# Kernel optimization log

Measured on AMD Instinct MI355X. Metric: run time of the kernel, lower is better.

## Reference

```python
import jax, jax.numpy as jnp
import numpy as np

N, E, G = 50000, 600000, 256
D, L, V = 128, 5, 128
BN_EPS = 1e-5


def setup_inputs() -> dict:
    key = jax.random.key(0)
    ks = jax.random.split(key, 24)
    x = jax.random.randint(ks[0], (N, 9), 0, V)
    edge_index = jax.random.randint(ks[1], (2, E), 0, N)
    edge_attr = jax.random.randint(ks[2], (E, 3), 0, V)
    batch = jnp.sort(jax.random.randint(ks[3], (N,), 0, G))
    s = 0.02
    inp = dict(
        x=x, edge_index=edge_index, edge_attr=edge_attr, batch=batch,
        atom_emb=jax.random.normal(ks[4], (9, V, D)) * s,
        bond_emb=jax.random.normal(ks[5], (L, 3, V, D)) * s,
        eps=jnp.zeros((L,)),
        W1=jax.random.normal(ks[6], (D, 2 * D)) * s, b1=jnp.zeros((2 * D,)),
        g1=jnp.ones((2 * D,)), be1=jnp.zeros((2 * D,)),
        W2=jax.random.normal(ks[7], (2 * D, D)) * s, b2=jnp.zeros((D,)),
        bn_g=jnp.ones((L, D)), bn_b=jnp.zeros((L, D)),
        fcW1=jax.random.normal(ks[8], (D, 1024)) * s, fcb1=jnp.zeros((1024,)),
        fcW2=jax.random.normal(ks[9], (1024, 1024)) * s, fcb2=jnp.zeros((1024,)),
        fcW3=jax.random.normal(ks[10], (1024, 512)) * s, fcb3=jnp.zeros((512,)),
        fcW4=jax.random.normal(ks[11], (512, 1)) * s, fcb4=jnp.zeros((1,)),
    )
    return inp


def _bn(h, g, b):
    # training-mode batchnorm (biased variance, as torch uses for normalization)
    m = h.mean(0)
    v = jnp.var(h, axis=0)
    return (h - m) * jax.lax.rsqrt(v + BN_EPS) * g + b


def _embed(tables, idx):
    # tables: [F, V, D], idx: [M, F] -> sum over F of table lookups -> [M, D]
    F = tables.shape[0]
    return tables[jnp.arange(F)[None, :], idx].sum(axis=1)


def reference(x, edge_index, edge_attr, batch, atom_emb, bond_emb, eps,
              W1, b1, g1, be1, W2, b2, bn_g, bn_b,
              fcW1, fcb1, fcW2, fcb2, fcW3, fcb3, fcW4, fcb4):
    src, dst = edge_index[0], edge_index[1]

    def mlp(h):
        z = jax.nn.relu(_bn(h @ W1 + b1, g1, be1))
        return z @ W2 + b2

    h = _embed(atom_emb, x)  # AtomEncoder: [N, D]
    h_sum = h  # JK='sum' accumulator
    for l in range(L):
        e = _embed(bond_emb[l], edge_attr)            # BondEncoder: [E, D]
        msg = jax.nn.relu(h[src] + e)                  # gather + elementwise
        agg = jax.ops.segment_sum(msg, dst, num_segments=N)  # scatter-add
        h = mlp((1.0 + eps[l]) * h + agg)
        h = _bn(h, bn_g[l], bn_b[l])
        if l < L - 1:
            h = jax.nn.relu(h)
        # dropout is identity in eval mode
        h_sum = h_sum + h

    # global mean pool over graphs
    sums = jax.ops.segment_sum(h_sum, batch, num_segments=G)
    cnts = jax.ops.segment_sum(jnp.ones((N,), h_sum.dtype), batch, num_segments=G)
    rep = sums / jnp.maximum(cnts, 1.0)[:, None]

    z = jax.nn.relu(rep @ fcW1 + fcb1)
    z = jax.nn.relu(z @ fcW2 + fcb2)
    z = jax.nn.relu(z @ fcW3 + fcb3)
    out = (z @ fcW4 + fcb4).squeeze(-1)  # [G]
    return out
```

## Files before the change

kernel.cpp:

```cpp
#include <hip/hip_runtime.h>

typedef unsigned short u16;
typedef unsigned int u32;
typedef __bf16 bf16x8 __attribute__((ext_vector_type(8)));
typedef float f32x4 __attribute__((ext_vector_type(4)));
typedef float f32x2 __attribute__((ext_vector_type(2)));

#define NN 50000
#define EE 600000
#define GG 256
#define LL 5
#define NB 196

__device__ __forceinline__ float b2f(u16 u) {
  unsigned int v = ((unsigned int)u) << 16;
  return __builtin_bit_cast(float, v);
}
__device__ __forceinline__ u16 f2b(float f) {
  unsigned int u = __builtin_bit_cast(unsigned int, f);
  u += 0x7FFFu + ((u >> 16) & 1u);
  return (u16)(u >> 16);
}
__device__ __forceinline__ f32x2 up2(u32 v) {
  f32x2 r;
  r.x = __builtin_bit_cast(float, v << 16);
  r.y = __builtin_bit_cast(float, v & 0xFFFF0000u);
  return r;
}
__device__ __forceinline__ f32x2 max0(f32x2 v) {
  f32x2 r;
  r.x = fmaxf(v.x, 0.f);
  r.y = fmaxf(v.y, 0.f);
  return r;
}

__global__ void k_detect(const u32* __restrict__ w, int* __restrict__ flag) {
  __shared__ int sh[256];
  u32 v = w[threadIdx.x];
  u32 lo = v & 0xFFFFu;
  u32 e = (lo >> 7) & 0xFFu;
  sh[threadIdx.x] = (e >= 0x60u && e <= 0x7Fu) ? 1 : 0;
  __syncthreads();
  for (int s = 128; s > 0; s >>= 1) {
    if (threadIdx.x < (unsigned)s) sh[threadIdx.x] += sh[threadIdx.x + s];
    __syncthreads();
  }
  if (threadIdx.x == 0) flag[0] = (sh[0] < 128) ? 1 : 0;
}

struct CvtArgs {
  const void* src[19];
  u16* dst[19];
  int cum[20];
};

__global__ void k_cvt_all(CvtArgs a, const int* __restrict__ flag) {
  int t = blockIdx.x * 256 + threadIdx.x;
  if (t >= a.cum[19]) return;
  int i = 0;
  while (t >= a.cum[i + 1]) ++i;
  int j = t - a.cum[i];
  if (flag[0]) a.dst[i][j] = f2b(((const float*)a.src[i])[j]);
  else a.dst[i][j] = ((const u16*)a.src[i])[j];
}

__global__ void k_tr(const u16* __restrict__ src, u16* __restrict__ dst, int K, int N) {
  __shared__ u16 t[32][33];
  const int kb = blockIdx.x * 32, nb = blockIdx.y * 32;
  const int tx = threadIdx.x & 31, ty = threadIdx.x >> 5;
#pragma unroll
  for (int i = ty; i < 32; i += 8) t[i][tx] = src[(kb + i) * N + nb + tx];
  __syncthreads();
#pragma unroll
  for (int i = ty; i < 32; i += 8) dst[(nb + i) * K + kb + tx] = t[tx][i];
}

__global__ void k_init(int* __restrict__ deg, float* __restrict__ rep,
                       float* __restrict__ bnbuf, int* __restrict__ gstart,
                       int* __restrict__ gend, float* __restrict__ c1b,
                       float* __restrict__ c0b) {
  int i = blockIdx.x * 256 + threadIdx.x;
  if (i < NN) deg[i] = 0;
  if (i < GG * 128) rep[i] = 0.f;
  if (i < 768) bnbuf[i] = 0.f;
  if (i < GG) { gstart[i] = 0; gend[i] = -1; }
  if (i < 128) { c1b[i] = 1.f; c0b[i] = 0.f; }
}

__global__ void k_deg(const int* __restrict__ ei, int* __restrict__ deg) {
  int e = blockIdx.x * 256 + threadIdx.x;
  if (e < EE) atomicAdd(&deg[ei[EE + e]], 1);
}

__global__ void k_scan1(const int* __restrict__ deg, int* __restrict__ rowp,
                        int* __restrict__ bsum) {
  __shared__ int sh[256];
  int i = blockIdx.x * 256 + threadIdx.x;
  int v = (i < NN) ? deg[i] : 0;
  sh[threadIdx.x] = v;
  __syncthreads();
  for (int s = 1; s < 256; s <<= 1) {
    int t = (threadIdx.x >= (unsigned)s) ? sh[threadIdx.x - s] : 0;
    __syncthreads();
    sh[threadIdx.x] += t;
    __syncthreads();
  }
  if (i < NN) rowp[i] = sh[threadIdx.x] - v;
  if (threadIdx.x == 255) bsum[blockIdx.x] = sh[255];
}

__global__ void k_scan2(int* __restrict__ bsum, int* __restrict__ boff) {
  __shared__ int sh[256];
  int v = (threadIdx.x < NB) ? bsum[threadIdx.x] : 0;
  sh[threadIdx.x] = v;
  __syncthreads();
  for (int s = 1; s < 256; s <<= 1) {
    int t = (threadIdx.x >= (unsigned)s) ? sh[threadIdx.x - s] : 0;
    __syncthreads();
    sh[threadIdx.x] += t;
    __syncthreads();
  }
  if (threadIdx.x < NB) boff[threadIdx.x] = sh[threadIdx.x] - v;
}

__global__ void k_scan3(int* __restrict__ rowp, const int* __restrict__ boff,
                        int* __restrict__ cursor) {
  int i = blockIdx.x * 256 + threadIdx.x;
  if (i < NN) {
    int r = rowp[i] + boff[blockIdx.x];
    rowp[i] = r;
    cursor[i] = r;
  }
  if (i == 0) rowp[NN] = EE;
}

__global__ void k_fill(const int* __restrict__ ei, const int* __restrict__ eattr,
                       int* __restrict__ cursor, uint2* __restrict__ epack) {
  int e = blockIdx.x * 256 + threadIdx.x;
  if (e < EE) {
    int d = ei[EE + e];
    int pos = atomicAdd(&cursor[d], 1);
    u32 src = (u32)ei[e];
    u32 a0 = (u32)eattr[e * 3], a1 = (u32)eattr[e * 3 + 1], a2 = (u32)eattr[e * 3 + 2];
    epack[pos] = make_uint2(src | (a0 << 16) | (a1 << 23), a2);
  }
}

__global__ void k_gb(const int* __restrict__ batch, int* __restrict__ gstart,
                     int* __restrict__ gend) {
  int n = blockIdx.x * 256 + threadIdx.x;
  if (n >= NN) return;
  int b = batch[n];
  if (n == 0 || batch[n - 1] != b) gstart[b] = n;
  if (n == NN - 1 || batch[n + 1] != b) gend[b] = n;
}

__global__ void k_atom(const int* __restrict__ x, const u16* __restrict__ aemb,
                       u16* __restrict__ hpre) {
  int idx = blockIdx.x * 256 + threadIdx.x;
  if (idx >= NN * 64) return;
  int n = idx >> 6, f2 = (idx & 63) << 1;
  float a0 = 0.f, a1 = 0.f;
#pragma unroll
  for (int j = 0; j < 9; ++j) {
    int xv = x[n * 9 + j];
    u32 v = *(const u32*)(aemb + (j * 128 + xv) * 128 + f2);
    a0 += b2f((u16)v);
    a1 += b2f((u16)(v >> 16));
  }
  u32 o = (u32)f2b(a0) | ((u32)f2b(a1) << 16);
  *(u32*)(hpre + n * 128 + f2) = o;
}

__global__ __launch_bounds__(256)
void k_pull(const u16* __restrict__ hpre, const float* __restrict__ cs1,
            const float* __restrict__ cs0, int relu_h, const int* __restrict__ rowp,
            const uint2* __restrict__ epack, const u16* __restrict__ bond,
            const u16* __restrict__ epsv, int layer, u16* __restrict__ amat) {
  const int lane = threadIdx.x & 63;
  const int node = blockIdx.x * 4 + (threadIdx.x >> 6);
  const int p0 = rowp[node], p1 = rowp[node + 1];
  const int lo = lane << 1;
  const u16* bondB = bond + 16384;
  const u16* bondC = bond + 32768;
  f32x2 c1v, c0v;
  c1v.x = cs1[lo]; c1v.y = cs1[lo + 1];
  c0v.x = cs0[lo]; c0v.y = cs0[lo + 1];
  auto act = [&](u32 v) -> f32x2 {
    f32x2 t = up2(v);
    t = t * c1v + c0v;
    if (relu_h) t = max0(t);
    return t;
  };
  f32x2 acc = {0.f, 0.f};
  int p = p0;
  for (; p + 4 <= p1; p += 4) {
    uint2 e0 = epack[p], e1 = epack[p + 1], e2 = epack[p + 2], e3 = epack[p + 3];
    u32 h0 = *(const u32*)(hpre + (size_t)(e0.x & 0xFFFFu) * 128 + lo);
    u32 h1 = *(const u32*)(hpre + (size_t)(e1.x & 0xFFFFu) * 128 + lo);
    u32 h2 = *(const u32*)(hpre + (size_t)(e2.x & 0xFFFFu) * 128 + lo);
    u32 h3 = *(const u32*)(hpre + (size_t)(e3.x & 0xFFFFu) * 128 + lo);
    u32 a0 = *(const u32*)(bond + ((e0.x >> 16) & 0x7Fu) * 128 + lo);
    u32 a1 = *(const u32*)(bond + ((e1.x >> 16) & 0x7Fu) * 128 + lo);
    u32 a2 = *(const u32*)(bond + ((e2.x >> 16) & 0x7Fu) * 128 + lo);
    u32 a3 = *(const u32*)(bond + ((e3.x >> 16) & 0x7Fu) * 128 + lo);
    u32 b0 = *(const u32*)(bondB + ((e0.x >> 23) & 0x7Fu) * 128 + lo);
    u32 b1 = *(const u32*)(bondB + ((e1.x >> 23) & 0x7Fu) * 128 + lo);
    u32 b2 = *(const u32*)(bondB + ((e2.x >> 23) & 0x7Fu) * 128 + lo);
    u32 b3 = *(const u32*)(bondB + ((e3.x >> 23) & 0x7Fu) * 128 + lo);
    u32 c0 = *(const u32*)(bondC + e0.y * 128 + lo);
    u32 c1 = *(const u32*)(bondC + e1.y * 128 + lo);
    u32 c2 = *(const u32*)(bondC + e2.y * 128 + lo);
    u32 c3 = *(const u32*)(bondC + e3.y * 128 + lo);
    acc += max0(act(h0) + up2(a0) + up2(b0) + up2(c0));
    acc += max0(act(h1) + up2(a1) + up2(b1) + up2(c1));
    acc += max0(act(h2) + up2(a2) + up2(b2) + up2(c2));
    acc += max0(act(h3) + up2(a3) + up2(b3) + up2(c3));
  }
  for (; p < p1; ++p) {
    uint2 e0 = epack[p];
    u32 h0 = *(const u32*)(hpre + (size_t)(e0.x & 0xFFFFu) * 128 + lo);
    u32 a0 = *(const u32*)(bond + ((e0.x >> 16) & 0x7Fu) * 128 + lo);
    u32 b0 = *(const u32*)(bondB + ((e0.x >> 23) & 0x7Fu) * 128 + lo);
    u32 c0 = *(const u32*)(bondC + e0.y * 128 + lo);
    acc += max0(act(h0) + up2(a0) + up2(b0) + up2(c0));
  }
  float epsf = 1.0f + b2f(epsv[layer]);
  u32 own = *(const u32*)(hpre + (size_t)node * 128 + lo);
  f32x2 ow = act(own);
  u32 o = (u32)f2b(epsf * ow.x + acc.x) | ((u32)f2b(epsf * ow.y + acc.y) << 16);
  *(u32*)(amat + (size_t)node * 128 + lo) = o;
}

__global__ __launch_bounds__(256, 2)
void k_gemm1(const u16* __restrict__ amat, const u16* __restrict__ w1t,
             const u16* __restrict__ b1, u16* __restrict__ z0,
             float* __restrict__ bnsum, float* __restrict__ bnsq) {
  __shared__ u16 As[128 * 72];
  __shared__ u16 Bs[128 * 72];
  __shared__ float colAcc[256];
  const int tid = threadIdx.x;
  const int r0 = blockIdx.x * 128;
  const int nc = blockIdx.y * 128;
  const int w = tid >> 6, lane = tid & 63, l15 = lane & 15, q = lane >> 4;
  const int wr = (w & 1) * 64, wc = (w >> 1) * 64;
  f32x4 acc[4][4];
#pragma unroll
  for (int i = 0; i < 4; ++i)
#pragma unroll
    for (int j = 0; j < 4; ++j) acc[i][j] = {0.f, 0.f, 0.f, 0.f};

#pragma unroll
  for (int ks = 0; ks < 2; ++ks) {
    const int k0 = ks * 64;
    for (int idx = tid; idx < 1024; idx += 256) {
      const int row = idx >> 3, c8 = (idx & 7) << 3;
      int gr = r0 + row; if (gr >= NN) gr = NN - 1;
      uint4 va = *(const uint4*)(amat + (size_t)gr * 128 + k0 + c8);
      *(uint4*)(As + row * 72 + c8) = va;
      uint4 vb = *(const uint4*)(w1t + (size_t)(nc + row) * 128 + k0 + c8);
      *(uint4*)(Bs + row * 72 + c8) = vb;
    }
    __syncthreads();
#pragma unroll
    for (int kk = 0; kk < 64; kk += 32) {
      const int kf = kk + q * 8;
      bf16x8 a[4], b[4];
#pragma unroll
      for (int i = 0; i < 4; ++i) a[i] = *(const bf16x8*)(As + (wr + i * 16 + l15) * 72 + kf);
#pragma unroll
      for (int j = 0; j < 4; ++j) b[j] = *(const bf16x8*)(Bs + (wc + j * 16 + l15) * 72 + kf);
#pragma unroll
      for (int i = 0; i < 4; ++i)
#pragma unroll
        for (int j = 0; j < 4; ++j)
          acc[i][j] = __builtin_amdgcn_mfma_f32_16x16x32_bf16(a[i], b[j], acc[i][j], 0, 0, 0);
    }
    __syncthreads();
  }
  colAcc[tid] = 0.f;
  __syncthreads();
#pragma unroll
  for (int j = 0; j < 4; ++j) {
    const int c = wc + j * 16 + l15;
    const float bias = b2f(b1[nc + c]);
    float ls = 0.f, lsq = 0.f;
#pragma unroll
    for (int i = 0; i < 4; ++i) {
      const int gr = r0 + wr + i * 16 + q * 4;
#pragma unroll
      for (int rg = 0; rg < 4; ++rg) {
        if (gr + rg < NN) {
          const float v = acc[i][j][rg] + bias;
          z0[(gr + rg) * 256 + nc + c] = f2b(v);
          ls += v;
          lsq += v * v;
        }
      }
    }
    atomicAdd(&colAcc[c], ls);
    atomicAdd(&colAcc[128 + c], lsq);
  }
  __syncthreads();
  if (tid < 128) {
    atomicAdd(&bnsum[nc + tid], colAcc[tid]);
    atomicAdd(&bnsq[nc + tid], colAcc[128 + tid]);
  }
}

__global__ void k_bnfin(float* __restrict__ bnsum, float* __restrict__ bnsq,
                        const u16* __restrict__ g, const u16* __restrict__ b,
                        float* __restrict__ c1, float* __restrict__ c0) {
  int t = threadIdx.x;
  float s = bnsum[t], q = bnsq[t];
  bnsum[t] = 0.f;
  bnsq[t] = 0.f;
  float m = s * (1.0f / NN);
  float var = q * (1.0f / NN) - m * m;
  float rs = rsqrtf(var + 1e-5f);
  float cc1 = rs * b2f(g[t]);
  c1[t] = cc1;
  c0[t] = b2f(b[t]) - m * cc1;
}

__global__ __launch_bounds__(256, 2)
void k_gemm2(const u16* __restrict__ z0, const float* __restrict__ c1,
             const float* __restrict__ c0, const u16* __restrict__ w2t,
             const u16* __restrict__ b2, u16* __restrict__ hpre,
             float* __restrict__ bnsum, float* __restrict__ bnsq) {
  __shared__ u16 As[128 * 72];
  __shared__ u16 Bs[128 * 72];
  __shared__ float colAcc[256];
  const int tid = threadIdx.x;
  const int r0 = blockIdx.x * 128;
  const int w = tid >> 6, lane = tid & 63, l15 = lane & 15, q = lane >> 4;
  const int wr = (w & 1) * 64, wc = (w >> 1) * 64;
  f32x4 acc[4][4];
#pragma unroll
  for (int i = 0; i < 4; ++i)
#pragma unroll
    for (int j = 0; j < 4; ++j) acc[i][j] = {0.f, 0.f, 0.f, 0.f};

#pragma unroll
  for (int ks = 0; ks < 4; ++ks) {
    const int k0 = ks * 64;
    for (int idx = tid; idx < 1024; idx += 256) {
      const int row = idx >> 3, c8 = (idx & 7) << 3;
      int gr = r0 + row; if (gr >= NN) gr = NN - 1;
      ushort4 z01 = *(const ushort4*)(z0 + (size_t)gr * 256 + k0 + c8);
      ushort4 z23 = *(const ushort4*)(z0 + (size_t)gr * 256 + k0 + c8 + 4);
      ushort4 o01, o23;
      {
        const int k = k0 + c8;
        o01.x = f2b(fmaxf(b2f(z01.x) * c1[k + 0] + c0[k + 0], 0.f));
        o01.y = f2b(fmaxf(b2f(z01.y) * c1[k + 1] + c0[k + 1], 0.f));
        o01.z = f2b(fmaxf(b2f(z01.z) * c1[k + 2] + c0[k + 2], 0.f));
        o01.w = f2b(fmaxf(b2f(z01.w) * c1[k + 3] + c0[k + 3], 0.f));
        o23.x = f2b(fmaxf(b2f(z23.x) * c1[k + 4] + c0[k + 4], 0.f));
        o23.y = f2b(fmaxf(b2f(z23.y) * c1[k + 5] + c0[k + 5], 0.f));
        o23.z = f2b(fmaxf(b2f(z23.z) * c1[k + 6] + c0[k + 6], 0.f));
        o23.w = f2b(fmaxf(b2f(z23.w) * c1[k + 7] + c0[k + 7], 0.f));
      }
      *(ushort4*)(As + row * 72 + c8) = o01;
      *(ushort4*)(As + row * 72 + c8 + 4) = o23;
      uint4 vb = *(const uint4*)(w2t + (size_t)row * 256 + k0 + c8);
      *(uint4*)(Bs + row * 72 + c8) = vb;
    }
    __syncthreads();
#pragma unroll
    for (int kk = 0; kk < 64; kk += 32) {
      const int kf = kk + q * 8;
      bf16x8 a[4], b[4];
#pragma unroll
      for (int i = 0; i < 4; ++i) a[i] = *(const bf16x8*)(As + (wr + i * 16 + l15) * 72 + kf);
#pragma unroll
      for (int j = 0; j < 4; ++j) b[j] = *(const bf16x8*)(Bs + (wc + j * 16 + l15) * 72 + kf);
#pragma unroll
      for (int i = 0; i < 4; ++i)
#pragma unroll
        for (int j = 0; j < 4; ++j)
          acc[i][j] = __builtin_amdgcn_mfma_f32_16x16x32_bf16(a[i], b[j], acc[i][j], 0, 0, 0);
    }
    __syncthreads();
  }
  colAcc[tid] = 0.f;
  __syncthreads();
#pragma unroll
  for (int j = 0; j < 4; ++j) {
    const int c = wc + j * 16 + l15;
    const float bias = b2f(b2[c]);
    float ls = 0.f, lsq = 0.f;
#pragma unroll
    for (int i = 0; i < 4; ++i) {
      const int gr = r0 + wr + i * 16 + q * 4;
#pragma unroll
      for (int rg = 0; rg < 4; ++rg) {
        if (gr + rg < NN) {
          const float v = acc[i][j][rg] + bias;
          hpre[(gr + rg) * 128 + c] = f2b(v);
          ls += v;
          lsq += v * v;
        }
      }
    }
    atomicAdd(&colAcc[c], ls);
    atomicAdd(&colAcc[128 + c], lsq);
  }
  __syncthreads();
  if (tid < 128) {
    atomicAdd(&bnsum[tid], colAcc[tid]);
    atomicAdd(&bnsq[tid], colAcc[128 + tid]);
  }
}

__global__ void k_poolseg(const u16* __restrict__ hpre, const float* __restrict__ cs1,
                          const float* __restrict__ cs0, int dorelu,
                          const int* __restrict__ gstart, const int* __restrict__ gend,
                          float* __restrict__ rep) {
  int g = blockIdx.x >> 2, part = blockIdx.x & 3, f = threadIdx.x;
  int r0 = gstart[g], r1 = gend[g] + 1;
  int len = r1 - r0;
  if (len <= 0) return;
  int chunk = (len + 3) >> 2;
  int s = r0 + part * chunk;
  int e = s + chunk; if (e > r1) e = r1;
  float cf1 = cs1[f], cf0 = cs0[f];
  float acc = 0.f;
  for (int r = s; r < e; ++r) {
    float v = b2f(hpre[r * 128 + f]) * cf1 + cf0;
    if (dorelu) v = fmaxf(v, 0.f);
    acc += v;
  }
  if (s < e) atomicAdd(&rep[g * 128 + f], acc);
}

__global__ void k_rep(float* __restrict__ rep, const int* __restrict__ gstart,
                      const int* __restrict__ gend, u16* __restrict__ repb) {
  int idx = blockIdx.x * 256 + threadIdx.x;
  int g = idx >> 7;
  int c = gend[g] - gstart[g] + 1;
  if (c < 1) c = 1;
  float v = rep[idx] / (float)c;
  rep[idx] = v;
  repb[idx] = f2b(v);
}

__global__ __launch_bounds__(256)
void k_fcg(const u16* __restrict__ A, const u16* __restrict__ Wt,
           const u16* __restrict__ bias, u16* __restrict__ out, int K, int N) {
  const int tid = threadIdx.x;
  const int r0 = blockIdx.x * 128;
  const int nc = blockIdx.y * 128;
  const int w = tid >> 6, lane = tid & 63, l15 = lane & 15, q = lane >> 4;
  const int wr = (w & 1) * 64, wc = (w >> 1) * 64;
  f32x4 acc[4][4];
#pragma unroll
  for (int i = 0; i < 4; ++i)
#pragma unroll
    for (int j = 0; j < 4; ++j) acc[i][j] = {0.f, 0.f, 0.f, 0.f};
  const int nkb = K >> 5;
  for (int kb = 0; kb < nkb; ++kb) {
    const int kf = kb * 32 + q * 8;
    bf16x8 a[4], b[4];
#pragma unroll
    for (int i = 0; i < 4; ++i)
      a[i] = *(const bf16x8*)(A + (size_t)(r0 + wr + i * 16 + l15) * K + kf);
#pragma unroll
    for (int j = 0; j < 4; ++j)
      b[j] = *(const bf16x8*)(Wt + (size_t)(nc + wc + j * 16 + l15) * K + kf);
#pragma unroll
    for (int i = 0; i < 4; ++i)
#pragma unroll
      for (int j = 0; j < 4; ++j)
        acc[i][j] = __builtin_amdgcn_mfma_f32_16x16x32_bf16(a[i], b[j], acc[i][j], 0, 0, 0);
  }
#pragma unroll
  for (int j = 0; j < 4; ++j) {
    const int c = nc + wc + j * 16 + l15;
    const float bv = b2f(bias[c]);
#pragma unroll
    for (int i = 0; i < 4; ++i) {
      const int gr = r0 + wr + i * 16 + q * 4;
#pragma unroll
      for (int rg = 0; rg < 4; ++rg)
        out[(gr + rg) * N + c] = f2b(fmaxf(acc[i][j][rg] + bv, 0.f));
    }
  }
}

__global__ void k_fc4(const u16* __restrict__ z, const u16* __restrict__ W,
                      const u16* __restrict__ bias, void* __restrict__ out,
                      const int* __restrict__ flag) {
  int g = blockIdx.x, lane = threadIdx.x;
  float acc = 0.f;
  for (int k = lane; k < 512; k += 64) acc += b2f(z[g * 512 + k]) * b2f(W[k]);
  for (int off = 32; off > 0; off >>= 1) acc += __shfl_down(acc, off);
  if (lane == 0) {
    float r = acc + b2f(bias[0]);
    if (flag[0]) ((float*)out)[g] = r;
    else ((u16*)out)[g] = f2b(r);
  }
}

extern "C" void kernel_launch(void* const* d_in, const int* in_sizes, int n_in,
                              void* d_out, int out_size, void* d_ws, size_t ws_size,
                              hipStream_t stream) {
  const int* x     = (const int*)d_in[0];
  const int* ei    = (const int*)d_in[1];
  const int* eattr = (const int*)d_in[2];
  const int* batch = (const int*)d_in[3];

  char* ws = (char*)d_ws;
  size_t off = 0;
  auto alloc = [&](size_t bytes) -> void* {
    void* p = ws + off;
    off += (bytes + 255) & ~(size_t)255;
    return p;
  };
  int* flag = (int*)alloc(256);
  u16* cvt[23];
  CvtArgs ca;
  ca.cum[0] = 0;
  for (int i = 4; i <= 22; ++i) {
    cvt[i] = (u16*)alloc((size_t)in_sizes[i] * 2);
    ca.src[i - 4] = d_in[i];
    ca.dst[i - 4] = cvt[i];
    ca.cum[i - 3] = ca.cum[i - 4] + in_sizes[i];
  }

  u16*   hpre   = (u16*)  alloc((size_t)NN * 128 * 2);
  u16*   amat   = (u16*)  alloc((size_t)NN * 128 * 2);
  u16*   z0     = (u16*)  alloc((size_t)NN * 256 * 2);
  u16*   w1t    = (u16*)  alloc(32768 * 2);
  u16*   w2t    = (u16*)  alloc(32768 * 2);
  u16*   ft1    = (u16*)  alloc((size_t)1024 * 128 * 2);
  u16*   ft2    = (u16*)  alloc((size_t)1024 * 1024 * 2);
  u16*   ft3    = (u16*)  alloc((size_t)512 * 1024 * 2);
  int*   deg    = (int*)  alloc((size_t)NN * 4);
  int*   cursor = (int*)  alloc((size_t)NN * 4);
  int*   rowp   = (int*)  alloc((size_t)(NN + 1) * 4);
  int*   bsum   = (int*)  alloc((size_t)NB * 4);
  int*   boff   = (int*)  alloc((size_t)NB * 4);
  uint2* epack  = (uint2*)alloc((size_t)EE * 8);
  float* bnbuf  = (float*)alloc(768 * 4);
  float* bnstat = (float*)alloc(768 * 4);
  float* rep    = (float*)alloc((size_t)GG * 128 * 4);
  u16*   repb   = (u16*)  alloc((size_t)GG * 128 * 2);
  int*   gstart = (int*)  alloc((size_t)GG * 4);
  int*   gend   = (int*)  alloc((size_t)GG * 4);
  u16*   fz1    = (u16*)  alloc((size_t)GG * 1024 * 2);
  u16*   fz2    = (u16*)  alloc((size_t)GG * 1024 * 2);
  u16*   fz3    = (u16*)  alloc((size_t)GG * 512 * 2);
  (void)ws_size; (void)n_in; (void)out_size;

  float* bn1sum = bnbuf;
  float* bn1sq  = bnbuf + 256;
  float* bn2sum = bnbuf + 512;
  float* bn2sq  = bnbuf + 640;
  float* c1a    = bnstat;
  float* c0a    = bnstat + 256;
  float* c1b    = bnstat + 512;
  float* c0b    = bnstat + 640;

  k_detect<<<1, 256, 0, stream>>>((const u32*)d_in[4], flag);
  {
    int total = ca.cum[19];
    k_cvt_all<<<(total + 255) / 256, 256, 0, stream>>>(ca, flag);
  }
  const u16 *aembc = cvt[4], *bembc = cvt[5], *epsc = cvt[6], *w1c = cvt[7],
            *b1c = cvt[8], *g1c = cvt[9], *be1c = cvt[10], *w2c = cvt[11],
            *b2c = cvt[12], *bngc = cvt[13], *bnbc = cvt[14], *fw1 = cvt[15],
            *fb1 = cvt[16], *fw2 = cvt[17], *fb2 = cvt[18], *fw3 = cvt[19],
            *fb3 = cvt[20], *fw4 = cvt[21], *fb4 = cvt[22];

  {
    dim3 t1(4, 8), t2(8, 4), t3(4, 32), t4(32, 32), t5(32, 16);
    k_tr<<<t1, 256, 0, stream>>>(w1c, w1t, 128, 256);
    k_tr<<<t2, 256, 0, stream>>>(w2c, w2t, 256, 128);
    k_tr<<<t3, 256, 0, stream>>>(fw1, ft1, 128, 1024);
    k_tr<<<t4, 256, 0, stream>>>(fw2, ft2, 1024, 1024);
    k_tr<<<t5, 256, 0, stream>>>(fw3, ft3, 1024, 512);
  }

  k_init<<<(NN + 255) / 256, 256, 0, stream>>>(deg, rep, bnbuf, gstart, gend, c1b, c0b);
  k_deg<<<(EE + 255) / 256, 256, 0, stream>>>(ei, deg);
  k_scan1<<<NB, 256, 0, stream>>>(deg, rowp, bsum);
  k_scan2<<<1, 256, 0, stream>>>(bsum, boff);
  k_scan3<<<NB, 256, 0, stream>>>(rowp, boff, cursor);
  k_fill<<<(EE + 255) / 256, 256, 0, stream>>>(ei, eattr, cursor, epack);
  k_gb<<<(NN + 255) / 256, 256, 0, stream>>>(batch, gstart, gend);
  k_atom<<<(NN * 64 + 255) / 256, 256, 0, stream>>>(x, aembc, hpre);
  k_poolseg<<<GG * 4, 128, 0, stream>>>(hpre, c1b, c0b, 0, gstart, gend, rep);

  const int gx = (NN + 127) / 128;
  for (int l = 0; l < LL; ++l) {
    k_pull<<<(NN + 3) / 4, 256, 0, stream>>>(hpre, c1b, c0b, (l > 0) ? 1 : 0, rowp, epack,
                                             bembc + (size_t)l * 3 * 128 * 128, epsc, l, amat);
    dim3 grid1(gx, 2);
    k_gemm1<<<grid1, 256, 0, stream>>>(amat, w1t, b1c, z0, bn1sum, bn1sq);
    k_bnfin<<<1, 256, 0, stream>>>(bn1sum, bn1sq, g1c, be1c, c1a, c0a);
    k_gemm2<<<gx, 256, 0, stream>>>(z0, c1a, c0a, w2t, b2c, hpre, bn2sum, bn2sq);
    k_bnfin<<<1, 128, 0, stream>>>(bn2sum, bn2sq, bngc + l * 128, bnbc + l * 128,
                                   c1b, c0b);
    k_poolseg<<<GG * 4, 128, 0, stream>>>(hpre, c1b, c0b, (l < LL - 1) ? 1 : 0,
                                          gstart, gend, rep);
  }

  k_rep<<<(GG * 128) / 256, 256, 0, stream>>>(rep, gstart, gend, repb);
  {
    dim3 g1(2, 8), g2(2, 8), g3(2, 4);
    k_fcg<<<g1, 256, 0, stream>>>(repb, ft1, fb1, fz1, 128, 1024);
    k_fcg<<<g2, 256, 0, stream>>>(fz1, ft2, fb2, fz2, 1024, 1024);
    k_fcg<<<g3, 256, 0, stream>>>(fz2, ft3, fb3, fz3, 1024, 512);
  }
  k_fc4<<<GG, 64, 0, stream>>>(fz3, fw4, fb4, d_out, flag);
}
```

Before: 914.2 us.

## Split pull edges across half-waves with wider loads; batch GEMM tile loads

```diff
diff --git a/kernel.cpp b/kernel.cpp
--- a/kernel.cpp
+++ b/kernel.cpp
@@ -178,58 +178,77 @@
             const uint2* __restrict__ epack, const u16* __restrict__ bond,
             const u16* __restrict__ epsv, int layer, u16* __restrict__ amat) {
   const int lane = threadIdx.x & 63;
+  const int half = lane >> 5;
   const int node = blockIdx.x * 4 + (threadIdx.x >> 6);
+  const int lo = (lane & 31) << 2;
   const int p0 = rowp[node], p1 = rowp[node + 1];
-  const int lo = lane << 1;
   const u16* bondB = bond + 16384;
   const u16* bondC = bond + 32768;
-  f32x2 c1v, c0v;
-  c1v.x = cs1[lo]; c1v.y = cs1[lo + 1];
-  c0v.x = cs0[lo]; c0v.y = cs0[lo + 1];
-  auto act = [&](u32 v) -> f32x2 {
-    f32x2 t = up2(v);
-    t = t * c1v + c0v;
+  f32x2 c1L, c1H, c0L, c0H;
+  c1L.x = cs1[lo];     c1L.y = cs1[lo + 1];
+  c1H.x = cs1[lo + 2]; c1H.y = cs1[lo + 3];
+  c0L.x = cs0[lo];     c0L.y = cs0[lo + 1];
+  c0H.x = cs0[lo + 2]; c0H.y = cs0[lo + 3];
+  auto actL = [&](u32 v) -> f32x2 {
+    f32x2 t = up2(v) * c1L + c0L;
     if (relu_h) t = max0(t);
     return t;
   };
-  f32x2 acc = {0.f, 0.f};
-  int p = p0;
-  for (; p + 4 <= p1; p += 4) {
-    uint2 e0 = epack[p], e1 = epack[p + 1], e2 = epack[p + 2], e3 = epack[p + 3];
-    u32 h0 = *(const u32*)(hpre + (size_t)(e0.x & 0xFFFFu) * 128 + lo);
-    u32 h1 = *(const u32*)(hpre + (size_t)(e1.x & 0xFFFFu) * 128 + lo);
-    u32 h2 = *(const u32*)(hpre + (size_t)(e2.x & 0xFFFFu) * 128 + lo);
-    u32 h3 = *(const u32*)(hpre + (size_t)(e3.x & 0xFFFFu) * 128 + lo);
-    u32 a0 = *(const u32*)(bond + ((e0.x >> 16) & 0x7Fu) * 128 + lo);
-    u32 a1 = *(const u32*)(bond + ((e1.x >> 16) & 0x7Fu) * 128 + lo);
-    u32 a2 = *(const u32*)(bond + ((e2.x >> 16) & 0x7Fu) * 128 + lo);
-    u32 a3 = *(const u32*)(bond + ((e3.x >> 16) & 0x7Fu) * 128 + lo);
-    u32 b0 = *(const u32*)(bondB + ((e0.x >> 23) & 0x7Fu) * 128 + lo);
-    u32 b1 = *(const u32*)(bondB + ((e1.x >> 23) & 0x7Fu) * 128 + lo);
-    u32 b2 = *(const u32*)(bondB + ((e2.x >> 23) & 0x7Fu) * 128 + lo);
-    u32 b3 = *(const u32*)(bondB + ((e3.x >> 23) & 0x7Fu) * 128 + lo);
-    u32 c0 = *(const u32*)(bondC + e0.y * 128 + lo);
-    u32 c1 = *(const u32*)(bondC + e1.y * 128 + lo);
-    u32 c2 = *(const u32*)(bondC + e2.y * 128 + lo);
-    u32 c3 = *(const u32*)(bondC + e3.y * 128 + lo);
-    acc += max0(act(h0) + up2(a0) + up2(b0) + up2(c0));
-    acc += max0(act(h1) + up2(a1) + up2(b1) + up2(c1));
-    acc += max0(act(h2) + up2(a2) + up2(b2) + up2(c2));
-    acc += max0(act(h3) + up2(a3) + up2(b3) + up2(c3));
-  }
-  for (; p < p1; ++p) {
+  auto actH = [&](u32 v) -> f32x2 {
+    f32x2 t = up2(v) * c1H + c0H;
+    if (relu_h) t = max0(t);
+    return t;
+  };
+  f32x2 accL = {0.f, 0.f}, accH = {0.f, 0.f};
+  int p = p0 + half;
+  for (; p < p1 - 6; p += 8) {
+    uint2 e0 = epack[p], e1 = epack[p + 2], e2 = epack[p + 4], e3 = epack[p + 6];
+    uint2 hx0 = *(const uint2*)(hpre + (size_t)(e0.x & 0xFFFFu) * 128 + lo);
+    uint2 hx1 = *(const uint2*)(hpre + (size_t)(e1.x & 0xFFFFu) * 128 + lo);
+    uint2 hx2 = *(const uint2*)(hpre + (size_t)(e2.x & 0xFFFFu) * 128 + lo);
+    uint2 hx3 = *(const uint2*)(hpre + (size_t)(e3.x & 0xFFFFu) * 128 + lo);
+    uint2 ax0 = *(const uint2*)(bond + ((e0.x >> 16) & 0x7Fu) * 128 + lo);
+    uint2 ax1 = *(const uint2*)(bond + ((e1.x >> 16) & 0x7Fu) * 128 + lo);
+    uint2 ax2 = *(const uint2*)(bond + ((e2.x >> 16) & 0x7Fu) * 128 + lo);
+    uint2 ax3 = *(const uint2*)(bond + ((e3.x >> 16) & 0x7Fu) * 128 + lo);
+    uint2 bx0 = *(const uint2*)(bondB + ((e0.x >> 23) & 0x7Fu) * 128 + lo);
+    uint2 bx1 = *(const uint2*)(bondB + ((e1.x >> 23) & 0x7Fu) * 128 + lo);
+    uint2 bx2 = *(const uint2*)(bondB + ((e2.x >> 23) & 0x7Fu) * 128 + lo);
+    uint2 bx3 = *(const uint2*)(bondB + ((e3.x >> 23) & 0x7Fu) * 128 + lo);
+    uint2 cx0 = *(const uint2*)(bondC + e0.y * 128 + lo);
+    uint2 cx1 = *(const uint2*)(bondC + e1.y * 128 + lo);
+    uint2 cx2 = *(const uint2*)(bondC + e2.y * 128 + lo);
+    uint2 cx3 = *(const uint2*)(bondC + e3.y * 128 + lo);
+    accL += max0(actL(hx0.x) + up2(ax0.x) + up2(bx0.x) + up2(cx0.x));
+    accH += max0(actH(hx0.y) + up2(ax0.y) + up2(bx0.y) + up2(cx0.y));
+    accL += max0(actL(hx1.x) + up2(ax1.x) + up2(bx1.x) + up2(cx1.x));
+    accH += max0(actH(hx1.y) + up2(ax1.y) + up2(bx1.y) + up2(cx1.y));
+    accL += max0(actL(hx2.x) + up2(ax2.x) + up2(bx2.x) + up2(cx2.x));
+    accH += max0(actH(hx2.y) + up2(ax2.y) + up2(bx2.y) + up2(cx2.y));
+    accL += max0(actL(hx3.x) + up2(ax3.x) + up2(bx3.x) + up2(cx3.x));
+    accH += max0(actH(hx3.y) + up2(ax3.y) + up2(bx3.y) + up2(cx3.y));
+  }
+  for (; p < p1; p += 2) {
     uint2 e0 = epack[p];
-    u32 h0 = *(const u32*)(hpre + (size_t)(e0.x & 0xFFFFu) * 128 + lo);
-    u32 a0 = *(const u32*)(bond + ((e0.x >> 16) & 0x7Fu) * 128 + lo);
-    u32 b0 = *(const u32*)(bondB + ((e0.x >> 23) & 0x7Fu) * 128 + lo);
-    u32 c0 = *(const u32*)(bondC + e0.y * 128 + lo);
-    acc += max0(act(h0) + up2(a0) + up2(b0) + up2(c0));
-  }
-  float epsf = 1.0f + b2f(epsv[layer]);
-  u32 own = *(const u32*)(hpre + (size_t)node * 128 + lo);
-  f32x2 ow = act(own);
-  u32 o = (u32)f2b(epsf * ow.x + acc.x) | ((u32)f2b(epsf * ow.y + acc.y) << 16);
-  *(u32*)(amat + (size_t)node * 128 + lo) = o;
+    uint2 hx0 = *(const uint2*)(hpre + (size_t)(e0.x & 0xFFFFu) * 128 + lo);
+    uint2 ax0 = *(const uint2*)(bond + ((e0.x >> 16) & 0x7Fu) * 128 + lo);
+    uint2 bx0 = *(const uint2*)(bondB + ((e0.x >> 23) & 0x7Fu) * 128 + lo);
+    uint2 cx0 = *(const uint2*)(bondC + e0.y * 128 + lo);
+    accL += max0(actL(hx0.x) + up2(ax0.x) + up2(bx0.x) + up2(cx0.x));
+    accH += max0(actH(hx0.y) + up2(ax0.y) + up2(bx0.y) + up2(cx0.y));
+  }
+  accL.x += __shfl_xor(accL.x, 32);
+  accL.y += __shfl_xor(accL.y, 32);
+  accH.x += __shfl_xor(accH.x, 32);
+  accH.y += __shfl_xor(accH.y, 32);
+  if (half == 0) {
+    float epsf = 1.0f + b2f(epsv[layer]);
+    uint2 own = *(const uint2*)(hpre + (size_t)node * 128 + lo);
+    f32x2 oL = actL(own.x), oH = actH(own.y);
+    u32 w0 = (u32)f2b(epsf * oL.x + accL.x) | ((u32)f2b(epsf * oL.y + accL.y) << 16);
+    u32 w1 = (u32)f2b(epsf * oH.x + accH.x) | ((u32)f2b(epsf * oH.y + accH.y) << 16);
+    *(uint2*)(amat + (size_t)node * 128 + lo) = make_uint2(w0, w1);
+  }
 }
 
 __global__ __launch_bounds__(256, 2)
@@ -244,6 +263,7 @@
   const int nc = blockIdx.y * 128;
   const int w = tid >> 6, lane = tid & 63, l15 = lane & 15, q = lane >> 4;
   const int wr = (w & 1) * 64, wc = (w >> 1) * 64;
+  const int srow = tid >> 3, sc8 = (tid & 7) << 3;
   f32x4 acc[4][4];
 #pragma unroll
   for (int i = 0; i < 4; ++i)
@@ -253,13 +273,19 @@
 #pragma unroll
   for (int ks = 0; ks < 2; ++ks) {
     const int k0 = ks * 64;
-    for (int idx = tid; idx < 1024; idx += 256) {
-      const int row = idx >> 3, c8 = (idx & 7) << 3;
+    uint4 va[4], vb[4];
+#pragma unroll
+    for (int t = 0; t < 4; ++t) {
+      const int row = srow + t * 32;
       int gr = r0 + row; if (gr >= NN) gr = NN - 1;
-      uint4 va = *(const uint4*)(amat + (size_t)gr * 128 + k0 + c8);
-      *(uint4*)(As + row * 72 + c8) = va;
-      uint4 vb = *(const uint4*)(w1t + (size_t)(nc + row) * 128 + k0 + c8);
-      *(uint4*)(Bs + row * 72 + c8) = vb;
+      va[t] = *(const uint4*)(amat + (size_t)gr * 128 + k0 + sc8);
+      vb[t] = *(const uint4*)(w1t + (size_t)(nc + row) * 128 + k0 + sc8);
+    }
+#pragma unroll
+    for (int t = 0; t < 4; ++t) {
+      const int row = srow + t * 32;
+      *(uint4*)(As + row * 72 + sc8) = va[t];
+      *(uint4*)(Bs + row * 72 + sc8) = vb[t];
     }
     __syncthreads();
 #pragma unroll
@@ -335,6 +361,7 @@
   const int r0 = blockIdx.x * 128;
   const int w = tid >> 6, lane = tid & 63, l15 = lane & 15, q = lane >> 4;
   const int wr = (w & 1) * 64, wc = (w >> 1) * 64;
+  const int srow = tid >> 3, sc8 = (tid & 7) << 3;
   f32x4 acc[4][4];
 #pragma unroll
   for (int i = 0; i < 4; ++i)
@@ -344,27 +371,35 @@
 #pragma unroll
   for (int ks = 0; ks < 4; ++ks) {
     const int k0 = ks * 64;
-    for (int idx = tid; idx < 1024; idx += 256) {
-      const int row = idx >> 3, c8 = (idx & 7) << 3;
+    const int kb = k0 + sc8;
+    uint4 vz[4], vb[4];
+#pragma unroll
+    for (int t = 0; t < 4; ++t) {
+      const int row = srow + t * 32;
       int gr = r0 + row; if (gr >= NN) gr = NN - 1;
-      ushort4 z01 = *(const ushort4*)(z0 + (size_t)gr * 256 + k0 + c8);
-      ushort4 z23 = *(const ushort4*)(z0 + (size_t)gr * 256 + k0 + c8 + 4);
-      ushort4 o01, o23;
-      {
-        const int k = k0 + c8;
-        o01.x = f2b(fmaxf(b2f(z01.x) * c1[k + 0] + c0[k + 0], 0.f));
-        o01.y = f2b(fmaxf(b2f(z01.y) * c1[k + 1] + c0[k + 1], 0.f));
-        o01.z = f2b(fmaxf(b2f(z01.z) * c1[k + 2] + c0[k + 2], 0.f));
-        o01.w = f2b(fmaxf(b2f(z01.w) * c1[k + 3] + c0[k + 3], 0.f));
-        o23.x = f2b(fmaxf(b2f(z23.x) * c1[k + 4] + c0[k + 4], 0.f));
-        o23.y = f2b(fmaxf(b2f(z23.y) * c1[k + 5] + c0[k + 5], 0.f));
-        o23.z = f2b(fmaxf(b2f(z23.z) * c1[k + 6] + c0[k + 6], 0.f));
-        o23.w = f2b(fmaxf(b2f(z23.w) * c1[k + 7] + c0[k + 7], 0.f));
+      vz[t] = *(const uint4*)(z0 + (size_t)gr * 256 + kb);
+      vb[t] = *(const uint4*)(w2t + (size_t)row * 256 + kb);
+    }
+    f32x2 fc1[4], fc0[4];
+#pragma unroll
+    for (int e = 0; e < 4; ++e) {
+      fc1[e].x = c1[kb + 2 * e];     fc1[e].y = c1[kb + 2 * e + 1];
+      fc0[e].x = c0[kb + 2 * e];     fc0[e].y = c0[kb + 2 * e + 1];
+    }
+#pragma unroll
+    for (int t = 0; t < 4; ++t) {
+      const int row = srow + t * 32;
+      u32 zw[4] = {vz[t].x, vz[t].y, vz[t].z, vz[t].w};
+      u32 ow[4];
+#pragma unroll
+      for (int e = 0; e < 4; ++e) {
+        f32x2 r = max0(up2(zw[e]) * fc1[e] + fc0[e]);
+        ow[e] = (u32)f2b(r.x) | ((u32)f2b(r.y) << 16);
       }
-      *(ushort4*)(As + row * 72 + c8) = o01;
-      *(ushort4*)(As + row * 72 + c8 + 4) = o23;
-      uint4 vb = *(const uint4*)(w2t + (size_t)row * 256 + k0 + c8);
-      *(uint4*)(Bs + row * 72 + c8) = vb;
+      uint4 oz;
+      oz.x = ow[0]; oz.y = ow[1]; oz.z = ow[2]; oz.w = ow[3];
+      *(uint4*)(As + row * 72 + sc8) = oz;
+      *(uint4*)(Bs + row * 72 + sc8) = vb[t];
     }
     __syncthreads();
 #pragma unroll
```

Result: slower. 993.5 us (+8.7%).
